# Performance work log

Hardware: AMD Instinct MI355X
Metric: run time of the kernel (lower is better)

## Reference

```python
import jax, jax.numpy as jnp
import numpy as np

NUM_GRAPHS = 64
NEG_SLOPE = 0.1


def gcn_conv(x, src, dst, W, b, num_nodes):
    h = x @ W  # [N, out]
    ones = jnp.ones(src.shape[0], dtype=x.dtype)
    deg = jax.ops.segment_sum(ones, dst, num_segments=num_nodes) + 1.0  # +1 self-loop
    dinv = jax.lax.rsqrt(deg)  # deg >= 1 always
    coef = dinv[src] * dinv[dst]  # [E]
    agg = jax.ops.segment_sum(h[src] * coef[:, None], dst, num_segments=num_nodes)
    # self-loop contribution: dinv[i]^2 * h[i]
    out = agg + h * (dinv * dinv)[:, None] + b
    return out


def leaky_relu(x):
    return jnp.where(x >= 0, x, NEG_SLOPE * x)


def global_mean_pool(x, batch, num_graphs):
    s = jax.ops.segment_sum(x, batch, num_segments=num_graphs)
    cnt = jax.ops.segment_sum(jnp.ones(x.shape[0], dtype=x.dtype), batch, num_segments=num_graphs)
    return s / jnp.maximum(cnt, 1.0)[:, None]


def setup_inputs() -> dict:
    key = jax.random.key(0)
    ks = jax.random.split(key, 10)
    N, E, D_IN, D_H, D_OUT, C = 50000, 600000, 128, 128, 128, 16
    x = jax.random.normal(ks[0], (N, D_IN), dtype=jnp.float32)
    edge_index = jax.random.randint(ks[1], (2, E), 0, N, dtype=jnp.int32)
    batch = jnp.sort(jax.random.randint(ks[2], (N,), 0, NUM_GRAPHS, dtype=jnp.int32))
    def glorot(k, shape):
        lim = np.sqrt(6.0 / (shape[0] + shape[1]))
        return jax.random.uniform(k, shape, jnp.float32, -lim, lim)
    W1 = glorot(ks[3], (D_IN, D_H))
    b1 = jnp.zeros((D_H,), jnp.float32)
    W2 = glorot(ks[4], (D_H, D_OUT))
    b2 = jnp.zeros((D_OUT,), jnp.float32)
    Wl = glorot(ks[5], (D_OUT, C))
    bl = jnp.zeros((C,), jnp.float32)
    return {"x": x, "edge_index": edge_index, "batch": batch,
            "W1": W1, "b1": b1, "W2": W2, "b2": b2, "Wl": Wl, "bl": bl}


def reference(x, edge_index, batch, W1, b1, W2, b2, Wl, bl):
    N = x.shape[0]
    src, dst = edge_index[0], edge_index[1]
    h = gcn_conv(x, src, dst, W1, b1, N)
    h = leaky_relu(h)
    h = gcn_conv(h, src, dst, W2, b2, N)
    h = leaky_relu(h)
    g = global_mean_pool(h, batch, NUM_GRAPHS)  # [G, D_OUT]
    # dropout p=0.2 is identity in eval mode
    return g @ Wl + bl
```

## Files before the change

### kernel.cpp

```cpp
#include <hip/hip_runtime.h>

#define D 128
#define NG 64
#define NC 16
#define NEG 0.1f

typedef __attribute__((ext_vector_type(8))) short bf16x8;
typedef __attribute__((ext_vector_type(4))) float f32x4;

__device__ __forceinline__ float bf2f(unsigned int u16) {
    union { unsigned int i; float f; } c;
    c.i = u16 << 16;
    return c.f;
}
__device__ __forceinline__ unsigned short f2bf(float f) {
    union { float f; unsigned int i; } c;
    c.f = f;
    unsigned int i = c.i;
    unsigned int r = (i + 0x7FFFu + ((i >> 16) & 1u)) >> 16;
    return (unsigned short)r;
}

__global__ __launch_bounds__(256) void prep_gemm1_kernel(
        const float* __restrict__ x, const float* __restrict__ W1,
        unsigned int* __restrict__ C, int gb,
        const float* __restrict__ W2, unsigned short* __restrict__ Wf2,
        float* __restrict__ pooled,
        const int* __restrict__ dst, int* __restrict__ deg, int E, int N) {
    __shared__ uint4 Ws[2048];
    int b = blockIdx.x;
    int tid = threadIdx.x;
    if (b < gb) {
        int w = tid >> 6, lane = tid & 63;
        int quad = lane >> 4, m16 = lane & 15;
        int rowstart = b * 64;
#pragma unroll
        for (int i = 0; i < 8; i++) {
            int fid = tid + 256 * i;
            int fm = fid & 15;
            int fquad = (fid >> 4) & 3;
            int fkc = (fid >> 6) & 3;
            int ft = fid >> 8;
            int n = ft * 16 + fm;
            int k0 = fkc * 32 + fquad * 8;
            unsigned short r[8];
#pragma unroll
            for (int j = 0; j < 8; j++) r[j] = f2bf(W1[(k0 + j) * 128 + n]);
            uint4 v;
            v.x = (unsigned int)r[0] | ((unsigned int)r[1] << 16);
            v.y = (unsigned int)r[2] | ((unsigned int)r[3] << 16);
            v.z = (unsigned int)r[4] | ((unsigned int)r[5] << 16);
            v.w = (unsigned int)r[6] | ((unsigned int)r[7] << 16);
            Ws[fid] = v;
        }

        int arow = rowstart + 16 * w + m16;
        bool valid = arow < N;
        bf16x8 af[4];
#pragma unroll
        for (int kc = 0; kc < 4; kc++) {
            float4 f0 = make_float4(0.f, 0.f, 0.f, 0.f), f1 = f0;
            if (valid) {
                const float4* p = (const float4*)(x + (size_t)arow * 128 + kc * 32 + quad * 8);
                f0 = p[0];
                f1 = p[1];
            }
            bf16x8 a;
            a[0] = (short)f2bf(f0.x); a[1] = (short)f2bf(f0.y);
            a[2] = (short)f2bf(f0.z); a[3] = (short)f2bf(f0.w);
            a[4] = (short)f2bf(f1.x); a[5] = (short)f2bf(f1.y);
            a[6] = (short)f2bf(f1.z); a[7] = (short)f2bf(f1.w);
            af[kc] = a;
        }
        __syncthreads();

        f32x4 acc[8];
#pragma unroll
        for (int t = 0; t < 8; t++) acc[t] = (f32x4){0.f, 0.f, 0.f, 0.f};
#pragma unroll
        for (int t = 0; t < 8; t++) {
#pragma unroll
            for (int kc = 0; kc < 4; kc++) {
                bf16x8 bh = *(const bf16x8*)&Ws[(((t * 4 + kc) * 4 + quad) * 16 + m16)];
                acc[t] = __builtin_amdgcn_mfma_f32_16x16x32_bf16(af[kc], bh, acc[t], 0, 0, 0);
            }
        }
#pragma unroll
        for (int t = 0; t < 8; t++) {
#pragma unroll
            for (int r = 0; r < 4; r++) {
                int row = rowstart + 16 * w + quad * 4 + r;
                unsigned int us = f2bf(acc[t][r]);
                unsigned int other = (unsigned int)__shfl_xor((int)us, 1);
                if (((m16 & 1) == 0) && row < N)
                    C[(size_t)row * 64 + t * 8 + (m16 >> 1)] = us | (other << 16);
            }
        }
    } else {
        int bb = b - gb;
        if (bb < 8) {
            int fid = bb * 256 + tid;
            int m = fid & 15;
            int quad = (fid >> 4) & 3;
            int kc = (fid >> 6) & 3;
            int t = fid >> 8;
            int n = t * 16 + m;
            int k0 = kc * 32 + quad * 8;
            unsigned short r[8];
#pragma unroll
            for (int j = 0; j < 8; j++) r[j] = f2bf(W2[(k0 + j) * 128 + n]);
            uint4 v;
            v.x = (unsigned int)r[0] | ((unsigned int)r[1] << 16);
            v.y = (unsigned int)r[2] | ((unsigned int)r[3] << 16);
            v.z = (unsigned int)r[4] | ((unsigned int)r[5] << 16);
            v.w = (unsigned int)r[6] | ((unsigned int)r[7] << 16);
            ((uint4*)Wf2)[fid] = v;
        } else if (bb < 40) {
            pooled[(bb - 8) * 256 + tid] = 0.f;
        } else {
            int e = (bb - 40) * 256 + tid;
            if (e < E) atomicAdd(&deg[dst[e]], 1);
        }
    }
}

__global__ void scan_block_kernel(const int* __restrict__ deg, int* __restrict__ scan1,
                                  int* __restrict__ blocksum, float* __restrict__ dinv, int N) {
    __shared__ int sm[256];
    int tid = threadIdx.x;
    int i = blockIdx.x * 256 + tid;
    int v = (i < N) ? deg[i] : 0;
    if (i < N) dinv[i] = 1.0f / sqrtf((float)v + 1.0f);
    sm[tid] = v;
    __syncthreads();
    for (int off = 1; off < 256; off <<= 1) {
        int t = (tid >= off) ? sm[tid - off] : 0;
        __syncthreads();
        sm[tid] += t;
        __syncthreads();
    }
    if (i < N) scan1[i] = sm[tid];
    if (tid == 255) blocksum[blockIdx.x] = sm[255];
}

__global__ void finalize_ptr_kernel(const int* __restrict__ deg, const int* __restrict__ scan1,
                                    const int* __restrict__ blocksum, int* __restrict__ ptr,
                                    int* __restrict__ fill, int nb, int N, int E) {
    __shared__ int sm[256];
    int tid = threadIdx.x;
    int v = (tid < nb) ? blocksum[tid] : 0;
    sm[tid] = v;
    __syncthreads();
    for (int off = 1; off < 256; off <<= 1) {
        int t = (tid >= off) ? sm[tid - off] : 0;
        __syncthreads();
        sm[tid] += t;
        __syncthreads();
    }
    int blockoff = (blockIdx.x > 0) ? sm[blockIdx.x - 1] : 0;
    int i = blockIdx.x * 256 + tid;
    if (i < N) {
        int p = scan1[i] - deg[i] + blockoff;
        ptr[i] = p;
        fill[i] = p;
        if (i == N - 1) ptr[N] = E;
    }
}

__global__ void scatter_kernel(const int* __restrict__ src, const int* __restrict__ dst,
                               int* __restrict__ fill, const float* __restrict__ dinv,
                               int2* __restrict__ csr_edge, int E) {
    int e = blockIdx.x * blockDim.x + threadIdx.x;
    if (e < E) {
        int d = dst[e];
        int s = src[e];
        int pos = atomicAdd(&fill[d], 1);
        float coef = dinv[s] * dinv[d];
        csr_edge[pos] = make_int2(s, __float_as_int(coef));
    }
}

#define ACC8(v, c)                                                         \
    a0 += bf2f((v).x & 0xffffu) * (c); a1 += bf2f((v).x >> 16) * (c);      \
    a2 += bf2f((v).y & 0xffffu) * (c); a3 += bf2f((v).y >> 16) * (c);      \
    a4 += bf2f((v).z & 0xffffu) * (c); a5 += bf2f((v).z >> 16) * (c);      \
    a6 += bf2f((v).w & 0xffffu) * (c); a7 += bf2f((v).w >> 16) * (c);

__global__ __launch_bounds__(256) void combine_gemm_kernel(
        const uint4* __restrict__ h4,
        const int* __restrict__ ptr,
        const int2* __restrict__ csr_edge,
        const float* __restrict__ dinv,
        const float* __restrict__ b,
        const uint4* __restrict__ Wf2,
        unsigned int* __restrict__ C,
        int N) {
    __shared__ int2 smeta[4][64];
    __shared__ unsigned int rowt[16 * 68];
    int wave = threadIdx.x >> 6;
    int lane = threadIdx.x & 63;
    int q = lane >> 4;
    int l16 = lane & 15;
    int bb = blockIdx.x * 16;
    int nb = bb + wave * 4;
    int node = nb + q;
    bool valid = node < N;

    if (nb < N) {
        int wlo = ptr[nb];
        int whi = ptr[min(nb + 4, N)];
        int lo = valid ? ptr[node] : 0;
        int hi = valid ? ptr[node + 1] : 0;

        float di = valid ? dinv[node] : 0.f;
        uint4 sv = valid ? h4[(size_t)node * 16 + l16] : make_uint4(0u, 0u, 0u, 0u);
        float4 bv0 = ((const float4*)b)[l16 * 2];
        float4 bv1 = ((const float4*)b)[l16 * 2 + 1];

        float a0 = 0.f, a1 = 0.f, a2 = 0.f, a3 = 0.f, a4 = 0.f, a5 = 0.f, a6 = 0.f, a7 = 0.f;

#pragma unroll 1
        for (int base = wlo; base < whi; base += 64) {
            if (base + lane < whi) smeta[wave][lane] = csr_edge[base + lane];
            int s = max(lo, base);
            int e = min(hi, base + 64);
            int j = s;
#pragma unroll 1
            for (; j + 3 < e; j += 4) {
                int k = j - base;
                int2 e0 = smeta[wave][k];
                int2 e1 = smeta[wave][k + 1];
                int2 e2 = smeta[wave][k + 2];
                int2 e3 = smeta[wave][k + 3];
                uint4 v0 = h4[(size_t)e0.x * 16 + l16];
                uint4 v1 = h4[(size_t)e1.x * 16 + l16];
                uint4 v2 = h4[(size_t)e2.x * 16 + l16];
                uint4 v3 = h4[(size_t)e3.x * 16 + l16];
                float c0 = __int_as_float(e0.y);
                float c1 = __int_as_float(e1.y);
                float c2 = __int_as_float(e2.y);
                float c3 = __int_as_float(e3.y);
                ACC8(v0, c0)
                ACC8(v1, c1)
                ACC8(v2, c2)
                ACC8(v3, c3)
            }
#pragma unroll 1
            for (; j < e; j++) {
                int k = j - base;
                int2 e0 = smeta[wave][k];
                uint4 v0 = h4[(size_t)e0.x * 16 + l16];
                float c0 = __int_as_float(e0.y);
                ACC8(v0, c0)
            }
        }

        if (valid) {
            float dd = di * di;
            float v0 = a0 + bf2f(sv.x & 0xffffu) * dd + bv0.x;
            float v1 = a1 + bf2f(sv.x >> 16) * dd + bv0.y;
            float v2 = a2 + bf2f(sv.y & 0xffffu) * dd + bv0.z;
            float v3 = a3 + bf2f(sv.y >> 16) * dd + bv0.w;
            float v4 = a4 + bf2f(sv.z & 0xffffu) * dd + bv1.x;
            float v5 = a5 + bf2f(sv.z >> 16) * dd + bv1.y;
            float v6 = a6 + bf2f(sv.w & 0xffffu) * dd + bv1.z;
            float v7 = a7 + bf2f(sv.w >> 16) * dd + bv1.w;
            v0 = (v0 >= 0.f) ? v0 : NEG * v0;
            v1 = (v1 >= 0.f) ? v1 : NEG * v1;
            v2 = (v2 >= 0.f) ? v2 : NEG * v2;
            v3 = (v3 >= 0.f) ? v3 : NEG * v3;
            v4 = (v4 >= 0.f) ? v4 : NEG * v4;
            v5 = (v5 >= 0.f) ? v5 : NEG * v5;
            v6 = (v6 >= 0.f) ? v6 : NEG * v6;
            v7 = (v7 >= 0.f) ? v7 : NEG * v7;
            unsigned int* p = &rowt[(wave * 4 + q) * 68 + l16 * 4];
            p[0] = (unsigned int)f2bf(v0) | ((unsigned int)f2bf(v1) << 16);
            p[1] = (unsigned int)f2bf(v2) | ((unsigned int)f2bf(v3) << 16);
            p[2] = (unsigned int)f2bf(v4) | ((unsigned int)f2bf(v5) << 16);
            p[3] = (unsigned int)f2bf(v6) | ((unsigned int)f2bf(v7) << 16);
        }
    }
    __syncthreads();

#pragma unroll
    for (int tt = 0; tt < 2; tt++) {
        int t = wave * 2 + tt;
        f32x4 acc = (f32x4){0.f, 0.f, 0.f, 0.f};
#pragma unroll
        for (int kc = 0; kc < 4; kc++) {
            bf16x8 a = *(const bf16x8*)&rowt[l16 * 68 + kc * 16 + q * 4];
            bf16x8 bh = *(const bf16x8*)&Wf2[((t * 4 + kc) * 4 + q) * 16 + l16];
            acc = __builtin_amdgcn_mfma_f32_16x16x32_bf16(a, bh, acc, 0, 0, 0);
        }
#pragma unroll
        for (int r = 0; r < 4; r++) {
            int row = bb + q * 4 + r;
            unsigned int us = f2bf(acc[r]);
            unsigned int other = (unsigned int)__shfl_xor((int)us, 1);
            if (((l16 & 1) == 0) && row < N)
                C[(size_t)row * 64 + t * 8 + (l16 >> 1)] = us | (other << 16);
        }
    }
}

__global__ __launch_bounds__(256) void combine_kernel(const uint4* __restrict__ h4,
                                                      const int* __restrict__ ptr,
                                                      const int2* __restrict__ csr_edge,
                                                      const float* __restrict__ dinv,
                                                      const float* __restrict__ b,
                                                      uint4* __restrict__ out4, int N) {
    __shared__ int2 smeta[4][64];
    int wave = threadIdx.x >> 6;
    int lane = threadIdx.x & 63;
    int q = lane >> 4;
    int l16 = lane & 15;
    int nb = blockIdx.x * 16 + wave * 4;
    if (nb >= N) return;
    int node = nb + q;
    bool valid = node < N;

    int wlo = ptr[nb];
    int whi = ptr[min(nb + 4, N)];
    int lo = valid ? ptr[node] : 0;
    int hi = valid ? ptr[node + 1] : 0;

    float di = valid ? dinv[node] : 0.f;
    uint4 sv = valid ? h4[(size_t)node * 16 + l16] : make_uint4(0u, 0u, 0u, 0u);
    float4 bv0 = ((const float4*)b)[l16 * 2];
    float4 bv1 = ((const float4*)b)[l16 * 2 + 1];

    float a0 = 0.f, a1 = 0.f, a2 = 0.f, a3 = 0.f, a4 = 0.f, a5 = 0.f, a6 = 0.f, a7 = 0.f;

#pragma unroll 1
    for (int base = wlo; base < whi; base += 64) {
        if (base + lane < whi) smeta[wave][lane] = csr_edge[base + lane];
        int s = max(lo, base);
        int e = min(hi, base + 64);
        int j = s;
#pragma unroll 1
        for (; j + 3 < e; j += 4) {
            int k = j - base;
            int2 e0 = smeta[wave][k];
            int2 e1 = smeta[wave][k + 1];
            int2 e2 = smeta[wave][k + 2];
            int2 e3 = smeta[wave][k + 3];
            uint4 v0 = h4[(size_t)e0.x * 16 + l16];
            uint4 v1 = h4[(size_t)e1.x * 16 + l16];
            uint4 v2 = h4[(size_t)e2.x * 16 + l16];
            uint4 v3 = h4[(size_t)e3.x * 16 + l16];
            float c0 = __int_as_float(e0.y);
            float c1 = __int_as_float(e1.y);
            float c2 = __int_as_float(e2.y);
            float c3 = __int_as_float(e3.y);
            ACC8(v0, c0)
            ACC8(v1, c1)
            ACC8(v2, c2)
            ACC8(v3, c3)
        }
#pragma unroll 1
        for (; j < e; j++) {
            int k = j - base;
            int2 e0 = smeta[wave][k];
            uint4 v0 = h4[(size_t)e0.x * 16 + l16];
            float c0 = __int_as_float(e0.y);
            ACC8(v0, c0)
        }
    }

    if (!valid) return;
    float dd = di * di;
    float v0 = a0 + bf2f(sv.x & 0xffffu) * dd + bv0.x;
    float v1 = a1 + bf2f(sv.x >> 16) * dd + bv0.y;
    float v2 = a2 + bf2f(sv.y & 0xffffu) * dd + bv0.z;
    float v3 = a3 + bf2f(sv.y >> 16) * dd + bv0.w;
    float v4 = a4 + bf2f(sv.z & 0xffffu) * dd + bv1.x;
    float v5 = a5 + bf2f(sv.z >> 16) * dd + bv1.y;
    float v6 = a6 + bf2f(sv.w & 0xffffu) * dd + bv1.z;
    float v7 = a7 + bf2f(sv.w >> 16) * dd + bv1.w;
    v0 = (v0 >= 0.f) ? v0 : NEG * v0;
    v1 = (v1 >= 0.f) ? v1 : NEG * v1;
    v2 = (v2 >= 0.f) ? v2 : NEG * v2;
    v3 = (v3 >= 0.f) ? v3 : NEG * v3;
    v4 = (v4 >= 0.f) ? v4 : NEG * v4;
    v5 = (v5 >= 0.f) ? v5 : NEG * v5;
    v6 = (v6 >= 0.f) ? v6 : NEG * v6;
    v7 = (v7 >= 0.f) ? v7 : NEG * v7;
    uint4 pv;
    pv.x = (unsigned int)f2bf(v0) | ((unsigned int)f2bf(v1) << 16);
    pv.y = (unsigned int)f2bf(v2) | ((unsigned int)f2bf(v3) << 16);
    pv.z = (unsigned int)f2bf(v4) | ((unsigned int)f2bf(v5) << 16);
    pv.w = (unsigned int)f2bf(v6) | ((unsigned int)f2bf(v7) << 16);
    out4[(size_t)node * 16 + l16] = pv;
}

#define PROWS 128
__global__ void pool_accum_kernel(const unsigned int* __restrict__ a2,
                                  const int* __restrict__ batch,
                                  float* __restrict__ pooled, int N) {
    int wave = threadIdx.x >> 6;
    int lane = threadIdx.x & 63;
    int start = blockIdx.x * PROWS;
    int end = start + PROWS;
    if (end > N) end = N;
    float s0 = 0.f, s1 = 0.f;
    int curg = -1;
    for (int r = start + wave; r < end; r += 4) {
        int g = batch[r];
        if (g != curg) {
            if (curg >= 0) {
                atomicAdd(&pooled[curg * D + 2 * lane], s0);
                atomicAdd(&pooled[curg * D + 2 * lane + 1], s1);
            }
            curg = g;
            s0 = 0.f;
            s1 = 0.f;
        }
        unsigned int v = a2[(size_t)r * 64 + lane];
        s0 += bf2f(v & 0xffffu);
        s1 += bf2f(v >> 16);
    }
    if (curg >= 0) {
        atomicAdd(&pooled[curg * D + 2 * lane], s0);
        atomicAdd(&pooled[curg * D + 2 * lane + 1], s1);
    }
}

__global__ void final_kernel(const float* __restrict__ pooled, const int* __restrict__ batch,
                             const float* __restrict__ Wl, const float* __restrict__ bl,
                             float* __restrict__ out, int N) {
    int t = blockIdx.x * blockDim.x + threadIdx.x;
    if (t >= NG * NC) return;
    int g = t >> 4, c = t & 15;
    int l = 0, h = N;
    while (l < h) { int m = (l + h) >> 1; if (batch[m] < g) l = m + 1; else h = m; }
    int lo = l;
    h = N;
    while (l < h) { int m = (l + h) >> 1; if (batch[m] < g + 1) l = m + 1; else h = m; }
    int cnt = l - lo;
    float inv = 1.0f / (float)(cnt > 0 ? cnt : 1);
    float dot = 0.f;
    for (int k = 0; k < D; k++) dot += pooled[g * D + k] * Wl[k * NC + c];
    out[t] = dot * inv + bl[c];
}

extern "C" void kernel_launch(void* const* d_in, const int* in_sizes, int n_in,
                              void* d_out, int out_size, void* d_ws, size_t ws_size,
                              hipStream_t stream) {
    const float* x = (const float*)d_in[0];
    const int* ei = (const int*)d_in[1];
    const int* batch = (const int*)d_in[2];
    const float* W1 = (const float*)d_in[3];
    const float* b1 = (const float*)d_in[4];
    const float* W2 = (const float*)d_in[5];
    const float* b2 = (const float*)d_in[6];
    const float* Wlin = (const float*)d_in[7];
    const float* bl = (const float*)d_in[8];
    float* out = (float*)d_out;

    int N = in_sizes[0] / D;
    int E = in_sizes[1] / 2;
    const int* src = ei;
    const int* dst = ei + E;

    float* ws = (float*)d_ws;
    size_t o = 0;
    unsigned int* bufA = (unsigned int*)(ws + o); o += (size_t)N * 64;
    unsigned int* bufB = (unsigned int*)(ws + o); o += (size_t)N * 64;
    int* deg = (int*)(ws + o);      o += N;
    int* fill = (int*)(ws + o);     o += N;
    float* dinv = ws + o;           o += N;
    int* scan1 = (int*)(ws + o);    o += N;
    int* blocksum = (int*)(ws + o); o += 256;
    int* csr_ptr = (int*)(ws + o);  o += (N + 4);
    int2* csr_edge = (int2*)(ws + o); o += (size_t)2 * E;
    float* pooled = ws + o;         o += NG * D;
    unsigned short* Wf2 = (unsigned short*)(ws + o); o += 8192;

    hipMemsetAsync(deg, 0, (size_t)N * sizeof(int), stream);

    int tb = 256;
    int nscan = (N + 255) / 256;
    int gblocks = (N + 63) / 64;
    int cblocks = (N + 15) / 16;
    int eblocks = (E + 255) / 256;

    prep_gemm1_kernel<<<gblocks + 40 + eblocks, 256, 0, stream>>>(
        x, W1, (unsigned int*)bufA, gblocks, W2, Wf2, pooled, dst, deg, E, N);
    scan_block_kernel<<<nscan, 256, 0, stream>>>(deg, scan1, blocksum, dinv, N);
    finalize_ptr_kernel<<<nscan, 256, 0, stream>>>(deg, scan1, blocksum, csr_ptr, fill,
                                                   nscan, N, E);
    scatter_kernel<<<(E + tb - 1) / tb, tb, 0, stream>>>(src, dst, fill, dinv,
                                                         csr_edge, E);

    combine_gemm_kernel<<<cblocks, 256, 0, stream>>>((const uint4*)bufA, csr_ptr, csr_edge,
                                                     dinv, b1, (const uint4*)Wf2,
                                                     (unsigned int*)bufB, N);
    combine_kernel<<<cblocks, 256, 0, stream>>>((const uint4*)bufB, csr_ptr, csr_edge,
                                                dinv, b2, (uint4*)bufA, N);
    pool_accum_kernel<<<(N + PROWS - 1) / PROWS, 256, 0, stream>>>(bufA, batch, pooled, N);
    final_kernel<<<(NG * NC + tb - 1) / tb, tb, 0, stream>>>(pooled, batch, Wlin, bl, out, N);
}
```

Baseline: 227.3 us.

## Fuse scan passes via decoupled lookback and merge pooling with final linear

Replaces the two-kernel block scan with a single kernel. Each block publishes its aggregate with a flag bit, and later blocks spin on the flags of all earlier blocks to get their offset. Pooling and the final linear layer are merged into one kernel with a block per graph, which sums its contiguous node range in shared memory instead of using global atomics. This removes two launches and the zeroing of pooled, but the lookback relies on all blocks being co-resident (196 blocks) and the pool now runs on only 64 blocks, which limits its parallelism.

After: 267.6 us. 1.18x slower.

```diff
diff --git a/kernel.cpp b/kernel.cpp
--- a/kernel.cpp
+++ b/kernel.cpp
@@ -25,7 +25,6 @@
         const float* __restrict__ x, const float* __restrict__ W1,
         unsigned int* __restrict__ C, int gb,
         const float* __restrict__ W2, unsigned short* __restrict__ Wf2,
-        float* __restrict__ pooled,
         const int* __restrict__ dst, int* __restrict__ deg, int E, int N) {
     __shared__ uint4 Ws[2048];
     int b = blockIdx.x;
@@ -115,20 +114,22 @@
             v.z = (unsigned int)r[4] | ((unsigned int)r[5] << 16);
             v.w = (unsigned int)r[6] | ((unsigned int)r[7] << 16);
             ((uint4*)Wf2)[fid] = v;
-        } else if (bb < 40) {
-            pooled[(bb - 8) * 256 + tid] = 0.f;
         } else {
-            int e = (bb - 40) * 256 + tid;
+            int e = (bb - 8) * 256 + tid;
             if (e < E) atomicAdd(&deg[dst[e]], 1);
         }
     }
 }
 
-__global__ void scan_block_kernel(const int* __restrict__ deg, int* __restrict__ scan1,
-                                  int* __restrict__ blocksum, float* __restrict__ dinv, int N) {
+__global__ __launch_bounds__(256) void scanfin_kernel(const int* __restrict__ deg,
+                                                      unsigned int* __restrict__ flagagg,
+                                                      int* __restrict__ ptr,
+                                                      int* __restrict__ fill,
+                                                      float* __restrict__ dinv, int N, int E) {
     __shared__ int sm[256];
     int tid = threadIdx.x;
-    int i = blockIdx.x * 256 + tid;
+    int blk = blockIdx.x;
+    int i = blk * 256 + tid;
     int v = (i < N) ? deg[i] : 0;
     if (i < N) dinv[i] = 1.0f / sqrtf((float)v + 1.0f);
     sm[tid] = v;
@@ -139,28 +140,27 @@
         sm[tid] += t;
         __syncthreads();
     }
-    if (i < N) scan1[i] = sm[tid];
-    if (tid == 255) blocksum[blockIdx.x] = sm[255];
-}
-
-__global__ void finalize_ptr_kernel(const int* __restrict__ deg, const int* __restrict__ scan1,
-                                    const int* __restrict__ blocksum, int* __restrict__ ptr,
-                                    int* __restrict__ fill, int nb, int N, int E) {
-    __shared__ int sm[256];
-    int tid = threadIdx.x;
-    int v = (tid < nb) ? blocksum[tid] : 0;
-    sm[tid] = v;
-    __syncthreads();
-    for (int off = 1; off < 256; off <<= 1) {
-        int t = (tid >= off) ? sm[tid - off] : 0;
+    int incl = sm[tid];
+    if (tid == 0)
+        atomicExch(&flagagg[blk], (unsigned int)sm[255] | 0x80000000u);
+    __syncthreads();
+    unsigned int a = 0;
+    if (tid < blk) {
+        unsigned int w;
+        do {
+            w = (unsigned int)atomicAdd((int*)&flagagg[tid], 0);
+        } while (!(w & 0x80000000u));
+        a = w & 0x7fffffffu;
+    }
+    sm[tid] = (int)a;
+    __syncthreads();
+    for (int off = 128; off > 0; off >>= 1) {
+        if (tid < off) sm[tid] += sm[tid + off];
         __syncthreads();
-        sm[tid] += t;
-        __syncthreads();
-    }
-    int blockoff = (blockIdx.x > 0) ? sm[blockIdx.x - 1] : 0;
-    int i = blockIdx.x * 256 + tid;
+    }
+    int blockoff = sm[0];
     if (i < N) {
-        int p = scan1[i] - deg[i] + blockoff;
+        int p = incl - v + blockoff;
         ptr[i] = p;
         fill[i] = p;
         if (i == N - 1) ptr[N] = E;
@@ -393,54 +393,41 @@
     out4[(size_t)node * 16 + l16] = pv;
 }
 
-#define PROWS 128
-__global__ void pool_accum_kernel(const unsigned int* __restrict__ a2,
-                                  const int* __restrict__ batch,
-                                  float* __restrict__ pooled, int N) {
-    int wave = threadIdx.x >> 6;
-    int lane = threadIdx.x & 63;
-    int start = blockIdx.x * PROWS;
-    int end = start + PROWS;
-    if (end > N) end = N;
-    float s0 = 0.f, s1 = 0.f;
-    int curg = -1;
-    for (int r = start + wave; r < end; r += 4) {
-        int g = batch[r];
-        if (g != curg) {
-            if (curg >= 0) {
-                atomicAdd(&pooled[curg * D + 2 * lane], s0);
-                atomicAdd(&pooled[curg * D + 2 * lane + 1], s1);
-            }
-            curg = g;
-            s0 = 0.f;
-            s1 = 0.f;
-        }
-        unsigned int v = a2[(size_t)r * 64 + lane];
-        s0 += bf2f(v & 0xffffu);
-        s1 += bf2f(v >> 16);
-    }
-    if (curg >= 0) {
-        atomicAdd(&pooled[curg * D + 2 * lane], s0);
-        atomicAdd(&pooled[curg * D + 2 * lane + 1], s1);
-    }
-}
-
-__global__ void final_kernel(const float* __restrict__ pooled, const int* __restrict__ batch,
-                             const float* __restrict__ Wl, const float* __restrict__ bl,
-                             float* __restrict__ out, int N) {
-    int t = blockIdx.x * blockDim.x + threadIdx.x;
-    if (t >= NG * NC) return;
-    int g = t >> 4, c = t & 15;
+__global__ __launch_bounds__(256) void poolfinal_kernel(const unsigned int* __restrict__ a2,
+                                                        const int* __restrict__ batch,
+                                                        const float* __restrict__ Wl,
+                                                        const float* __restrict__ bl,
+                                                        float* __restrict__ out, int N) {
+    __shared__ float psum[4][128];
+    __shared__ float pl[128];
+    int g = blockIdx.x;
+    int tid = threadIdx.x;
+    int wave = tid >> 6, lane = tid & 63;
     int l = 0, h = N;
     while (l < h) { int m = (l + h) >> 1; if (batch[m] < g) l = m + 1; else h = m; }
     int lo = l;
     h = N;
     while (l < h) { int m = (l + h) >> 1; if (batch[m] < g + 1) l = m + 1; else h = m; }
-    int cnt = l - lo;
-    float inv = 1.0f / (float)(cnt > 0 ? cnt : 1);
-    float dot = 0.f;
-    for (int k = 0; k < D; k++) dot += pooled[g * D + k] * Wl[k * NC + c];
-    out[t] = dot * inv + bl[c];
+    int hi = l;
+    int cnt = hi - lo;
+
+    float s0 = 0.f, s1 = 0.f;
+    for (int r = lo + wave; r < hi; r += 4) {
+        unsigned int v = a2[(size_t)r * 64 + lane];
+        s0 += bf2f(v & 0xffffu);
+        s1 += bf2f(v >> 16);
+    }
+    psum[wave][2 * lane] = s0;
+    psum[wave][2 * lane + 1] = s1;
+    __syncthreads();
+    if (tid < 128) pl[tid] = psum[0][tid] + psum[1][tid] + psum[2][tid] + psum[3][tid];
+    __syncthreads();
+    if (tid < NC) {
+        float inv = 1.0f / (float)(cnt > 0 ? cnt : 1);
+        float dot = 0.f;
+        for (int k = 0; k < D; k++) dot += pl[k] * Wl[k * NC + tid];
+        out[g * NC + tid] = dot * inv + bl[tid];
+    }
 }
 
 extern "C" void kernel_launch(void* const* d_in, const int* in_sizes, int n_in,
@@ -467,16 +454,14 @@
     unsigned int* bufA = (unsigned int*)(ws + o); o += (size_t)N * 64;
     unsigned int* bufB = (unsigned int*)(ws + o); o += (size_t)N * 64;
     int* deg = (int*)(ws + o);      o += N;
+    unsigned int* flagagg = (unsigned int*)(ws + o); o += 256;
     int* fill = (int*)(ws + o);     o += N;
     float* dinv = ws + o;           o += N;
-    int* scan1 = (int*)(ws + o);    o += N;
-    int* blocksum = (int*)(ws + o); o += 256;
     int* csr_ptr = (int*)(ws + o);  o += (N + 4);
     int2* csr_edge = (int2*)(ws + o); o += (size_t)2 * E;
-    float* pooled = ws + o;         o += NG * D;
     unsigned short* Wf2 = (unsigned short*)(ws + o); o += 8192;
 
-    hipMemsetAsync(deg, 0, (size_t)N * sizeof(int), stream);
+    hipMemsetAsync(deg, 0, ((size_t)N + 256) * sizeof(int), stream);
 
     int tb = 256;
     int nscan = (N + 255) / 256;
@@ -484,19 +469,15 @@
     int cblocks = (N + 15) / 16;
     int eblocks = (E + 255) / 256;
 
-    prep_gemm1_kernel<<<gblocks + 40 + eblocks, 256, 0, stream>>>(
-        x, W1, (unsigned int*)bufA, gblocks, W2, Wf2, pooled, dst, deg, E, N);
-    scan_block_kernel<<<nscan, 256, 0, stream>>>(deg, scan1, blocksum, dinv, N);
-    finalize_ptr_kernel<<<nscan, 256, 0, stream>>>(deg, scan1, blocksum, csr_ptr, fill,
-                                                   nscan, N, E);
+    prep_gemm1_kernel<<<gblocks + 8 + eblocks, 256, 0, stream>>>(
+        x, W1, (unsigned int*)bufA, gblocks, W2, Wf2, dst, deg, E, N);
+    scanfin_kernel<<<nscan, 256, 0, stream>>>(deg, flagagg, csr_ptr, fill, dinv, N, E);
     scatter_kernel<<<(E + tb - 1) / tb, tb, 0, stream>>>(src, dst, fill, dinv,
                                                          csr_edge, E);
-
     combine_gemm_kernel<<<cblocks, 256, 0, stream>>>((const uint4*)bufA, csr_ptr, csr_edge,
                                                      dinv, b1, (const uint4*)Wf2,
                                                      (unsigned int*)bufB, N);
     combine_kernel<<<cblocks, 256, 0, stream>>>((const uint4*)bufB, csr_ptr, csr_edge,
                                                 dinv, b2, (uint4*)bufA, N);
-    pool_accum_kernel<<<(N + PROWS - 1) / PROWS, 256, 0, stream>>>(bufA, batch, pooled, N);
-    final_kernel<<<(NG * NC + tb - 1) / tb, tb, 0, stream>>>(pooled, batch, Wlin, bl, out, N);
-}
+    poolfinal_kernel<<<NG, 256, 0, stream>>>(bufA, batch, Wlin, bl, out, N);
+}
```
